# Kernel tuning notes

Measured on AMD Instinct MI355X. Metric: run time of the kernel, lower is better.

The kernel has to match this reference:

```python
import jax, jax.numpy as jnp
import numpy as np

NUM_HEADS = 16
D_MODEL = 1024
TEMPERATURE = D_MODEL ** 0.5  # note: module uses d_model**0.5, not head_dim**0.5


def setup_inputs() -> dict:
    key = jax.random.key(0)
    ks = jax.random.split(key, 8)
    B, T, D = 2, 2048, D_MODEL
    q = jax.random.normal(ks[0], (B, T, D), dtype=jnp.float32)
    k = jax.random.normal(ks[1], (B, T, D), dtype=jnp.float32)
    v = jax.random.normal(ks[2], (B, T, D), dtype=jnp.float32)
    # causal mask (tril) as suggested by the module docstring
    mask = jnp.tril(jnp.ones((T, T), dtype=bool))
    s = 1.0 / np.sqrt(D)
    Wq = jax.random.normal(ks[3], (D, D), dtype=jnp.float32) * s
    Wk = jax.random.normal(ks[4], (D, D), dtype=jnp.float32) * s
    Wv = jax.random.normal(ks[5], (D, D), dtype=jnp.float32) * s
    Wc = jax.random.normal(ks[6], (D, D), dtype=jnp.float32) * s
    return {"q": q, "k": k, "v": v, "Wq": Wq, "Wk": Wk, "Wv": Wv, "Wc": Wc, "mask": mask}


def reference(q, k, v, Wq, Wk, Wv, Wc, mask):
    B, T, D = q.shape
    H = NUM_HEADS
    hd = D // H
    # torch Linear (no bias): y = x @ W.T ; then split heads -> [B,H,T,hd]
    def proj(x, W):
        return (x @ W.T).reshape(B, T, H, hd).transpose(0, 2, 1, 3)
    qh, kh, vh = proj(q, Wq), proj(k, Wk), proj(v, Wv)
    # scores [B,H,T,T]
    scores = jnp.einsum("bhqd,bhkd->bhqk", qh / TEMPERATURE, kh)
    scores = jnp.where(mask, scores, -jnp.inf)
    attention = jax.nn.softmax(scores, axis=-1)  # dropout = identity (eval)
    out = jnp.einsum("bhqk,bhkd->bhqd", attention, vh)
    out = out.transpose(0, 2, 1, 3).reshape(B, T, D)
    out = out @ Wc.T  # combine projection; dropout = identity (eval)
    return (out, attention)
```

## Files before the change

kernel.cpp:

```cpp
#include <hip/hip_runtime.h>
#include <stdint.h>

typedef unsigned short u16;
typedef __bf16 bf16x8 __attribute__((ext_vector_type(8)));
typedef float f32x4 __attribute__((ext_vector_type(4)));

#define MFMA16(a, b, c) __builtin_amdgcn_mfma_f32_16x16x32_bf16((a), (b), (c), 0, 0, 0)

__device__ __forceinline__ u16 f2bf(float f) {
  union { __bf16 h; u16 u; } v;
  v.h = (__bf16)f;
  return v.u;
}

__device__ __forceinline__ float expf_c(float x) {
  return __expf(fmaxf(x, -80.0f));
}

struct Cvt6Args {
  const float* s0; const float* s1; const float* s2;
  const float* s3; const float* s4; const float* s5;
  u16* d0; u16* d1; u16* d2; u16* d3; u16* d4; u16* d5;
};

__global__ __launch_bounds__(256) void cvt6(Cvt6Args a) {
  const int z = blockIdx.y;
  const float* s; u16* d; int n8;
  if (z == 0)      { s = a.s0; d = a.d0; n8 = (4 * 1024 * 1024) / 8; }
  else if (z == 1) { s = a.s1; d = a.d1; n8 = (4 * 1024 * 1024) / 8; }
  else if (z == 2) { s = a.s2; d = a.d2; n8 = (4 * 1024 * 1024) / 8; }
  else if (z == 3) { s = a.s3; d = a.d3; n8 = (1024 * 1024) / 8; }
  else if (z == 4) { s = a.s4; d = a.d4; n8 = (1024 * 1024) / 8; }
  else             { s = a.s5; d = a.d5; n8 = (1024 * 1024) / 8; }
  const int i = blockIdx.x * 256 + threadIdx.x;
  if (i >= n8) return;
  float4 f0 = ((const float4*)s)[2 * i];
  float4 f1 = ((const float4*)s)[2 * i + 1];
  ushort4 h0, h1;
  h0.x = f2bf(f0.x); h0.y = f2bf(f0.y); h0.z = f2bf(f0.z); h0.w = f2bf(f0.w);
  h1.x = f2bf(f1.x); h1.y = f2bf(f1.y); h1.z = f2bf(f1.z); h1.w = f2bf(f1.w);
  ((ushort4*)d)[2 * i] = h0;
  ((ushort4*)d)[2 * i + 1] = h1;
}

__global__ __launch_bounds__(256) void cvt_one(const float* __restrict__ s,
                                               u16* __restrict__ d) {
  const int i = blockIdx.x * 256 + threadIdx.x;
  if (i >= (1024 * 1024) / 8) return;
  float4 f0 = ((const float4*)s)[2 * i];
  float4 f1 = ((const float4*)s)[2 * i + 1];
  ushort4 h0, h1;
  h0.x = f2bf(f0.x); h0.y = f2bf(f0.y); h0.z = f2bf(f0.z); h0.w = f2bf(f0.w);
  h1.x = f2bf(f1.x); h1.y = f2bf(f1.y); h1.z = f2bf(f1.z); h1.w = f2bf(f1.w);
  ((ushort4*)d)[2 * i] = h0;
  ((ushort4*)d)[2 * i + 1] = h1;
}

__device__ __forceinline__ void gemm_core(const u16* __restrict__ X,
                                          const u16* __restrict__ W,
                                          void* __restrict__ Yv, float scale,
                                          int omode) {
  __shared__ __align__(16) u16 lA[128 * 40];
  __shared__ __align__(16) u16 lB[128 * 40];
  const int tid = threadIdx.x;
  const int lane = tid & 63, w = tid >> 6;
  const int l15 = lane & 15, quad = lane >> 4;
  const int wm = (w >> 1) * 64, wn = (w & 1) * 64;
  const int m0 = blockIdx.x * 128, n0 = blockIdx.y * 128;

  f32x4 acc[4][4];
#pragma unroll
  for (int m = 0; m < 4; ++m)
#pragma unroll
    for (int n = 0; n < 4; ++n) acc[m][n] = (f32x4){0.f, 0.f, 0.f, 0.f};

  const int brow = tid >> 2, bseg = (tid & 3) * 8;

  for (int kk = 0; kk < 1024; kk += 32) {
    __syncthreads();
#pragma unroll
    for (int p = 0; p < 2; ++p) {
      int row = p * 64 + brow;
      *(uint4*)&lA[row * 40 + bseg] =
          *(const uint4*)&X[(size_t)(m0 + row) * 1024 + kk + bseg];
      *(uint4*)&lB[row * 40 + bseg] =
          *(const uint4*)&W[(size_t)(n0 + row) * 1024 + kk + bseg];
    }
    __syncthreads();
    bf16x8 af[4], bfr[4];
#pragma unroll
    for (int m = 0; m < 4; ++m)
      af[m] = *(const bf16x8*)&lA[(wm + m * 16 + l15) * 40 + quad * 8];
#pragma unroll
    for (int n = 0; n < 4; ++n)
      bfr[n] = *(const bf16x8*)&lB[(wn + n * 16 + l15) * 40 + quad * 8];
#pragma unroll
    for (int m = 0; m < 4; ++m)
#pragma unroll
      for (int n = 0; n < 4; ++n) acc[m][n] = MFMA16(af[m], bfr[n], acc[m][n]);
  }

  if (omode == 0) {
    u16* Y = (u16*)Yv;
#pragma unroll
    for (int m = 0; m < 4; ++m) {
      int grow0 = m0 + wm + m * 16 + quad * 4;
#pragma unroll
      for (int n = 0; n < 4; ++n) {
        int gcol = n0 + wn + n * 16 + l15;
#pragma unroll
        for (int r = 0; r < 4; ++r)
          Y[(size_t)(grow0 + r) * 1024 + gcol] = f2bf(acc[m][n][r] * scale);
      }
    }
  } else if (omode == 1) {
    u16* Y = (u16*)Yv;
#pragma unroll
    for (int m = 0; m < 4; ++m) {
      int grow0 = m0 + wm + m * 16 + quad * 4;
      int bb = grow0 >> 11, t = grow0 & 2047;
#pragma unroll
      for (int n = 0; n < 4; ++n) {
        int gcol = n0 + wn + n * 16 + l15;
        int hh = gcol >> 6, e = gcol & 63;
        ushort4 pk;
        pk.x = f2bf(acc[m][n][0]);
        pk.y = f2bf(acc[m][n][1]);
        pk.z = f2bf(acc[m][n][2]);
        pk.w = f2bf(acc[m][n][3]);
        *(ushort4*)&Y[((size_t)((bb * 16 + hh) * 64 + e)) * 2048 + t] = pk;
      }
    }
  } else {
    float* Y = (float*)Yv;
#pragma unroll
    for (int m = 0; m < 4; ++m) {
      int grow0 = m0 + wm + m * 16 + quad * 4;
#pragma unroll
      for (int n = 0; n < 4; ++n) {
        int gcol = n0 + wn + n * 16 + l15;
#pragma unroll
        for (int r = 0; r < 4; ++r)
          Y[(size_t)(grow0 + r) * 1024 + gcol] = acc[m][n][r] * scale;
      }
    }
  }
}

struct QKVArgs {
  const u16* X0; const u16* X1; const u16* X2;
  const u16* W0; const u16* W1; const u16* W2;
  void* Y0; void* Y1; void* Y2;
  float s0, s1, s2;
};

__global__ __launch_bounds__(256, 2) void proj_qkv(QKVArgs a) {
  const u16* X; const u16* W; void* Y; float sc; int om;
  if (blockIdx.z == 0)      { X = a.X0; W = a.W0; Y = a.Y0; sc = a.s0; om = 0; }
  else if (blockIdx.z == 1) { X = a.X1; W = a.W1; Y = a.Y1; sc = a.s1; om = 0; }
  else                      { X = a.X2; W = a.W2; Y = a.Y2; sc = a.s2; om = 1; }
  gemm_core(X, W, Y, sc, om);
}

__global__ __launch_bounds__(256, 2) void proj_out(const u16* __restrict__ Xv,
                                                   const u16* __restrict__ W,
                                                   void* __restrict__ Yv) {
  gemm_core(Xv, W, Yv, 1.0f, 2);
}

__global__ __launch_bounds__(256, 3) void attn_kernel(const u16* Qb,
                                                      const u16* __restrict__ Kb,
                                                      const u16* __restrict__ Vt,
                                                      float* __restrict__ attnF,
                                                      u16* Ob,
                                                      float* __restrict__ rowInv) {
  __shared__ __align__(16) u16 lK[64 * 72];
  __shared__ __align__(16) u16 lV[64 * 72];
  __shared__ __align__(16) u16 lP[4][16 * 72];

  const int bid = blockIdx.x;
  const int qt = bid & 31, bh = bid >> 5;
  const int b = bh >> 4, h = bh & 15;
  const int q0 = qt * 64;
  const int tid = threadIdx.x;
  const int w = tid >> 6, lane = tid & 63;
  const int l15 = lane & 15, quad = lane >> 4;

  {
    const int kz0 = q0 + 64;
    if (kz0 < 2048) {
      int r = tid >> 2;
      size_t base = ((size_t)bh * 2048 + q0 + r) * 2048;
      uint4 z = {0, 0, 0, 0};
      for (int c = kz0 + (tid & 3) * 4; c < 2048; c += 16)
        *(uint4*)&attnF[base + c] = z;
    }
  }

  const size_t qrowbase = (size_t)(b * 2048 + q0 + w * 16 + l15) * 1024 + h * 64;
  const bf16x8 aq0 = *(const bf16x8*)&Qb[qrowbase + quad * 8];
  const bf16x8 aq1 = *(const bf16x8*)&Qb[qrowbase + 32 + quad * 8];

  const int qglob0 = q0 + w * 16 + quad * 4;
  const int srow = tid >> 3, sseg = (tid & 7) * 8;

  float lpart[4];
  f32x4 o[4];
#pragma unroll
  for (int i = 0; i < 4; ++i) lpart[i] = 0.f;
#pragma unroll
  for (int n = 0; n < 4; ++n) o[n] = (f32x4){0.f, 0.f, 0.f, 0.f};

  size_t arow[4];
#pragma unroll
  for (int i = 0; i < 4; ++i)
    arow[i] = ((size_t)bh * 2048 + qglob0 + i) * 2048;

  for (int c = 0; c <= qt; ++c) {
    const int k0 = c * 64;
    __syncthreads();
#pragma unroll
    for (int p = 0; p < 2; ++p) {
      int rr = p * 32 + srow;
      *(uint4*)&lK[rr * 72 + sseg] =
          *(const uint4*)&Kb[(size_t)(b * 2048 + k0 + rr) * 1024 + h * 64 + sseg];
      *(uint4*)&lV[rr * 72 + sseg] =
          *(const uint4*)&Vt[((size_t)bh * 64 + rr) * 2048 + k0 + sseg];
    }
    __syncthreads();
    f32x4 s[4];
#pragma unroll
    for (int n = 0; n < 4; ++n) {
      s[n] = (f32x4){0.f, 0.f, 0.f, 0.f};
      bf16x8 bk0 = *(const bf16x8*)&lK[(n * 16 + l15) * 72 + quad * 8];
      bf16x8 bk1 = *(const bf16x8*)&lK[(n * 16 + l15) * 72 + 32 + quad * 8];
      s[n] = MFMA16(aq0, bk0, s[n]);
      s[n] = MFMA16(aq1, bk1, s[n]);
    }
    const bool diag = (c == qt);
#pragma unroll
    for (int n = 0; n < 4; ++n) {
      int key = k0 + n * 16 + l15;
#pragma unroll
      for (int i = 0; i < 4; ++i) {
        float p = expf_c(s[n][i]);
        if (diag && key > qglob0 + i) p = 0.f;
        lpart[i] += p;
        lP[w][(quad * 4 + i) * 72 + n * 16 + l15] = f2bf(p);
        attnF[arow[i] + key] = p;
      }
    }
#pragma unroll
    for (int kkk = 0; kkk < 2; ++kkk) {
      bf16x8 ap = *(const bf16x8*)&lP[w][l15 * 72 + kkk * 32 + quad * 8];
#pragma unroll
      for (int n = 0; n < 4; ++n) {
        bf16x8 bv = *(const bf16x8*)&lV[(n * 16 + l15) * 72 + kkk * 32 + quad * 8];
        o[n] = MFMA16(ap, bv, o[n]);
      }
    }
  }

  float invl[4];
#pragma unroll
  for (int i = 0; i < 4; ++i) {
    float l = lpart[i];
#pragma unroll
    for (int off = 1; off < 16; off <<= 1) l += __shfl_xor(l, off);
    invl[i] = 1.0f / fmaxf(l, 1e-30f);
    if (l15 == 0) rowInv[bh * 2048 + qglob0 + i] = invl[i];
  }

#pragma unroll
  for (int n = 0; n < 4; ++n)
#pragma unroll
    for (int i = 0; i < 4; ++i) {
      float ov = o[n][i] * invl[i];
      if (!(ov == ov)) ov = 0.f;
      lP[w][(quad * 4 + i) * 72 + n * 16 + l15] = f2bf(ov);
    }
  {
    int prow = lane >> 3, pseg = (lane & 7) * 8;
#pragma unroll
    for (int p2 = 0; p2 < 2; ++p2) {
      int rr = p2 * 8 + prow;
      *(uint4*)&Ob[(size_t)(b * 2048 + q0 + w * 16 + rr) * 1024 + h * 64 + pseg] =
          *(const uint4*)&lP[w][rr * 72 + pseg];
    }
  }
}

__global__ __launch_bounds__(256) void rescale_attn(float* __restrict__ attnF,
                                                    const float* __restrict__ rowInv) {
  const int bh = blockIdx.x;
  const int pg = blockIdx.y;
  const int pr = threadIdx.x >> 4;
  const int ln = threadIdx.x & 15;
  const int rp = pg * 16 + pr;
  const size_t bhbase = (size_t)bh * 2048 * 2048;
#pragma unroll
  for (int sel = 0; sel < 2; ++sel) {
    const int t = sel ? (2047 - rp) : rp;
    const float inv = rowInv[bh * 2048 + t];
    float* row = attnF + bhbase + (size_t)t * 2048;
    const int end = t + 1;
    for (int c = ln * 4; c < end; c += 64) {
      float4 p = *(float4*)&row[c];
      p.x *= inv; p.y *= inv; p.z *= inv; p.w *= inv;
      *(float4*)&row[c] = p;
    }
  }
}

extern "C" void kernel_launch(void* const* d_in, const int* in_sizes, int n_in,
                              void* d_out, int out_size, void* d_ws, size_t ws_size,
                              hipStream_t stream) {
  const float* q  = (const float*)d_in[0];
  const float* k  = (const float*)d_in[1];
  const float* v  = (const float*)d_in[2];
  const float* Wq = (const float*)d_in[3];
  const float* Wk = (const float*)d_in[4];
  const float* Wv = (const float*)d_in[5];
  const float* Wc = (const float*)d_in[6];

  float* outF  = (float*)d_out;
  float* attnF = outF + (size_t)4096 * 1024;

  const size_t BUF  = (size_t)4096 * 1024;
  const size_t WBUF = (size_t)1024 * 1024;
  const size_t INVL_BYTES = (size_t)65536 * sizeof(float);
  u16* ws = (u16*)d_ws;
  const bool big_ws = ws_size >= 4 * BUF * sizeof(u16) + INVL_BYTES;

  u16 *Qb, *Kb, *Vt, *Ob;
  float* rowInv;
  if (big_ws) {
    Qb = ws; Kb = ws + BUF; Vt = ws + 2 * BUF; Ob = ws + 3 * BUF;
    rowInv = (float*)(ws + 4 * BUF);
  } else {
    Qb = (u16*)outF; Ob = (u16*)outF + BUF; Kb = ws; Vt = ws + BUF;
    rowInv = (float*)(ws + 2 * BUF);
  }

  u16* qbf  = (u16*)attnF;
  u16* kbf  = qbf  + BUF;
  u16* vbf  = kbf  + BUF;
  u16* wqbf = vbf  + BUF;
  u16* wkbf = wqbf + WBUF;
  u16* wvbf = wkbf + WBUF;
  u16* wcbf = Vt;

  dim3 blk(256, 1, 1);

  Cvt6Args ca;
  ca.s0 = q;    ca.s1 = k;    ca.s2 = v;
  ca.s3 = Wq;   ca.s4 = Wk;   ca.s5 = Wv;
  ca.d0 = qbf;  ca.d1 = kbf;  ca.d2 = vbf;
  ca.d3 = wqbf; ca.d4 = wkbf; ca.d5 = wvbf;
  cvt6<<<dim3(2048, 6), blk, 0, stream>>>(ca);

  QKVArgs a;
  a.X0 = qbf;  a.X1 = kbf;  a.X2 = vbf;
  a.W0 = wqbf; a.W1 = wkbf; a.W2 = wvbf;
  a.Y0 = Qb; a.Y1 = Kb; a.Y2 = Vt;
  a.s0 = 0.03125f;
  a.s1 = 1.0f; a.s2 = 1.0f;
  proj_qkv<<<dim3(32, 8, 3), blk, 0, stream>>>(a);
  attn_kernel<<<dim3(1024), blk, 0, stream>>>(Qb, Kb, Vt, attnF, Ob, rowInv);

  cvt_one<<<dim3(512), blk, 0, stream>>>(Wc, wcbf);

  const u16* gemm_src = Ob;
  if (!big_ws) {
    hipMemcpyAsync(ws, Ob, BUF * sizeof(u16), hipMemcpyDeviceToDevice, stream);
    gemm_src = ws;
  }
  proj_out<<<dim3(32, 8), blk, 0, stream>>>(gemm_src, wcbf, outF);
  rescale_attn<<<dim3(32, 64), blk, 0, stream>>>(attnF, rowInv);
}
```

Before: 906.1 us.

## Two-pass attention: compute row sums first, write normalized probabilities directly

The attention kernel now makes a first pass over the causal key tiles to compute the softmax denominators, then a second pass that recomputes the scores and writes already-normalized probabilities. This removes the separate rescale kernel, which re-read and re-wrote the whole lower-triangular attention matrix. The QK MFMA operands are swapped so each lane holds four consecutive keys of one query row, enabling float4 stores to the attention output. K and V tiles are now read directly from global memory instead of being staged in LDS, which drops the block barriers but may increase global traffic and doubles the QK compute.

```diff
diff --git a/kernel.cpp b/kernel.cpp
--- a/kernel.cpp
+++ b/kernel.cpp
@@ -168,14 +168,11 @@
   gemm_core(Xv, W, Yv, 1.0f, 2);
 }
 
-__global__ __launch_bounds__(256, 3) void attn_kernel(const u16* Qb,
+__global__ __launch_bounds__(256, 3) void attn_kernel(const u16* __restrict__ Qb,
                                                       const u16* __restrict__ Kb,
                                                       const u16* __restrict__ Vt,
                                                       float* __restrict__ attnF,
-                                                      u16* Ob,
-                                                      float* __restrict__ rowInv) {
-  __shared__ __align__(16) u16 lK[64 * 72];
-  __shared__ __align__(16) u16 lV[64 * 72];
+                                                      u16* __restrict__ Ob) {
   __shared__ __align__(16) u16 lP[4][16 * 72];
 
   const int bid = blockIdx.x;
@@ -185,6 +182,7 @@
   const int tid = threadIdx.x;
   const int w = tid >> 6, lane = tid & 63;
   const int l15 = lane & 15, quad = lane >> 4;
+  const f32x4 ZERO4 = {0.f, 0.f, 0.f, 0.f};
 
   {
     const int kz0 = q0 + 64;
@@ -197,87 +195,97 @@
     }
   }
 
-  const size_t qrowbase = (size_t)(b * 2048 + q0 + w * 16 + l15) * 1024 + h * 64;
+  const int qrow = q0 + w * 16 + l15;
+  const size_t qrowbase = (size_t)(b * 2048 + qrow) * 1024 + h * 64;
   const bf16x8 aq0 = *(const bf16x8*)&Qb[qrowbase + quad * 8];
   const bf16x8 aq1 = *(const bf16x8*)&Qb[qrowbase + 32 + quad * 8];
 
-  const int qglob0 = q0 + w * 16 + quad * 4;
-  const int srow = tid >> 3, sseg = (tid & 7) * 8;
-
-  float lpart[4];
-  f32x4 o[4];
-#pragma unroll
-  for (int i = 0; i < 4; ++i) lpart[i] = 0.f;
-#pragma unroll
-  for (int n = 0; n < 4; ++n) o[n] = (f32x4){0.f, 0.f, 0.f, 0.f};
-
-  size_t arow[4];
-#pragma unroll
-  for (int i = 0; i < 4; ++i)
-    arow[i] = ((size_t)bh * 2048 + qglob0 + i) * 2048;
-
+  const int kq = quad * 4;
+  const size_t kb_base = (size_t)b * 2048 * 1024 + h * 64;
+
+  float lacc = 0.f;
   for (int c = 0; c <= qt; ++c) {
     const int k0 = c * 64;
-    __syncthreads();
-#pragma unroll
-    for (int p = 0; p < 2; ++p) {
-      int rr = p * 32 + srow;
-      *(uint4*)&lK[rr * 72 + sseg] =
-          *(const uint4*)&Kb[(size_t)(b * 2048 + k0 + rr) * 1024 + h * 64 + sseg];
-      *(uint4*)&lV[rr * 72 + sseg] =
-          *(const uint4*)&Vt[((size_t)bh * 64 + rr) * 2048 + k0 + sseg];
-    }
-    __syncthreads();
     f32x4 s[4];
 #pragma unroll
     for (int n = 0; n < 4; ++n) {
-      s[n] = (f32x4){0.f, 0.f, 0.f, 0.f};
-      bf16x8 bk0 = *(const bf16x8*)&lK[(n * 16 + l15) * 72 + quad * 8];
-      bf16x8 bk1 = *(const bf16x8*)&lK[(n * 16 + l15) * 72 + 32 + quad * 8];
-      s[n] = MFMA16(aq0, bk0, s[n]);
-      s[n] = MFMA16(aq1, bk1, s[n]);
+      const size_t krow = kb_base + (size_t)(k0 + n * 16 + l15) * 1024;
+      bf16x8 bk0 = *(const bf16x8*)&Kb[krow + quad * 8];
+      bf16x8 bk1 = *(const bf16x8*)&Kb[krow + 32 + quad * 8];
+      s[n] = MFMA16(bk0, aq0, ZERO4);
+      s[n] = MFMA16(bk1, aq1, s[n]);
+    }
+    if (c == qt) {
+#pragma unroll
+      for (int n = 0; n < 4; ++n) {
+        const int keyb = k0 + n * 16 + kq;
+#pragma unroll
+        for (int i = 0; i < 4; ++i)
+          lacc += (keyb + i > qrow) ? 0.f : expf_c(s[n][i]);
+      }
+    } else {
+#pragma unroll
+      for (int n = 0; n < 4; ++n)
+#pragma unroll
+        for (int i = 0; i < 4; ++i) lacc += expf_c(s[n][i]);
+    }
+  }
+  lacc += __shfl_xor(lacc, 16);
+  lacc += __shfl_xor(lacc, 32);
+  const float invl = 1.0f / fmaxf(lacc, 1e-30f);
+
+  f32x4 o[4];
+#pragma unroll
+  for (int n = 0; n < 4; ++n) o[n] = ZERO4;
+  const size_t arow = ((size_t)bh * 2048 + qrow) * 2048;
+  u16* lPw = lP[w];
+
+  for (int c = 0; c <= qt; ++c) {
+    const int k0 = c * 64;
+    f32x4 s[4];
+#pragma unroll
+    for (int n = 0; n < 4; ++n) {
+      const size_t krow = kb_base + (size_t)(k0 + n * 16 + l15) * 1024;
+      bf16x8 bk0 = *(const bf16x8*)&Kb[krow + quad * 8];
+      bf16x8 bk1 = *(const bf16x8*)&Kb[krow + 32 + quad * 8];
+      s[n] = MFMA16(bk0, aq0, ZERO4);
+      s[n] = MFMA16(bk1, aq1, s[n]);
     }
     const bool diag = (c == qt);
 #pragma unroll
     for (int n = 0; n < 4; ++n) {
-      int key = k0 + n * 16 + l15;
+      const int keyb = k0 + n * 16 + kq;
 #pragma unroll
       for (int i = 0; i < 4; ++i) {
-        float p = expf_c(s[n][i]);
-        if (diag && key > qglob0 + i) p = 0.f;
-        lpart[i] += p;
-        lP[w][(quad * 4 + i) * 72 + n * 16 + l15] = f2bf(p);
-        attnF[arow[i] + key] = p;
-      }
+        float p = expf_c(s[n][i]) * invl;
+        if (diag && keyb + i > qrow) p = 0.f;
+        s[n][i] = p;
+      }
+      *(f32x4*)&attnF[arow + keyb] = s[n];
+      ushort4 pk;
+      pk.x = f2bf(s[n][0]); pk.y = f2bf(s[n][1]);
+      pk.z = f2bf(s[n][2]); pk.w = f2bf(s[n][3]);
+      *(ushort4*)&lPw[l15 * 72 + n * 16 + kq] = pk;
     }
 #pragma unroll
     for (int kkk = 0; kkk < 2; ++kkk) {
-      bf16x8 ap = *(const bf16x8*)&lP[w][l15 * 72 + kkk * 32 + quad * 8];
-#pragma unroll
-      for (int n = 0; n < 4; ++n) {
-        bf16x8 bv = *(const bf16x8*)&lV[(n * 16 + l15) * 72 + kkk * 32 + quad * 8];
+      bf16x8 ap = *(const bf16x8*)&lPw[l15 * 72 + kkk * 32 + quad * 8];
+#pragma unroll
+      for (int n = 0; n < 4; ++n) {
+        const size_t vrow = ((size_t)(bh * 64 + n * 16 + l15)) * 2048;
+        bf16x8 bv = *(const bf16x8*)&Vt[vrow + k0 + kkk * 32 + quad * 8];
         o[n] = MFMA16(ap, bv, o[n]);
       }
     }
   }
 
-  float invl[4];
-#pragma unroll
-  for (int i = 0; i < 4; ++i) {
-    float l = lpart[i];
-#pragma unroll
-    for (int off = 1; off < 16; off <<= 1) l += __shfl_xor(l, off);
-    invl[i] = 1.0f / fmaxf(l, 1e-30f);
-    if (l15 == 0) rowInv[bh * 2048 + qglob0 + i] = invl[i];
-  }
-
 #pragma unroll
   for (int n = 0; n < 4; ++n)
 #pragma unroll
     for (int i = 0; i < 4; ++i) {
-      float ov = o[n][i] * invl[i];
+      float ov = o[n][i];
       if (!(ov == ov)) ov = 0.f;
-      lP[w][(quad * 4 + i) * 72 + n * 16 + l15] = f2bf(ov);
+      lPw[(quad * 4 + i) * 72 + n * 16 + l15] = f2bf(ov);
     }
   {
     int prow = lane >> 3, pseg = (lane & 7) * 8;
@@ -285,29 +293,7 @@
     for (int p2 = 0; p2 < 2; ++p2) {
       int rr = p2 * 8 + prow;
       *(uint4*)&Ob[(size_t)(b * 2048 + q0 + w * 16 + rr) * 1024 + h * 64 + pseg] =
-          *(const uint4*)&lP[w][rr * 72 + pseg];
-    }
-  }
-}
-
-__global__ __launch_bounds__(256) void rescale_attn(float* __restrict__ attnF,
-                                                    const float* __restrict__ rowInv) {
-  const int bh = blockIdx.x;
-  const int pg = blockIdx.y;
-  const int pr = threadIdx.x >> 4;
-  const int ln = threadIdx.x & 15;
-  const int rp = pg * 16 + pr;
-  const size_t bhbase = (size_t)bh * 2048 * 2048;
-#pragma unroll
-  for (int sel = 0; sel < 2; ++sel) {
-    const int t = sel ? (2047 - rp) : rp;
-    const float inv = rowInv[bh * 2048 + t];
-    float* row = attnF + bhbase + (size_t)t * 2048;
-    const int end = t + 1;
-    for (int c = ln * 4; c < end; c += 64) {
-      float4 p = *(float4*)&row[c];
-      p.x *= inv; p.y *= inv; p.z *= inv; p.w *= inv;
-      *(float4*)&row[c] = p;
+          *(const uint4*)&lPw[rr * 72 + pseg];
     }
   }
 }
@@ -328,18 +314,14 @@
 
   const size_t BUF  = (size_t)4096 * 1024;
   const size_t WBUF = (size_t)1024 * 1024;
-  const size_t INVL_BYTES = (size_t)65536 * sizeof(float);
   u16* ws = (u16*)d_ws;
-  const bool big_ws = ws_size >= 4 * BUF * sizeof(u16) + INVL_BYTES;
+  const bool big_ws = ws_size >= 4 * BUF * sizeof(u16);
 
   u16 *Qb, *Kb, *Vt, *Ob;
-  float* rowInv;
   if (big_ws) {
     Qb = ws; Kb = ws + BUF; Vt = ws + 2 * BUF; Ob = ws + 3 * BUF;
-    rowInv = (float*)(ws + 4 * BUF);
   } else {
     Qb = (u16*)outF; Ob = (u16*)outF + BUF; Kb = ws; Vt = ws + BUF;
-    rowInv = (float*)(ws + 2 * BUF);
   }
 
   u16* qbf  = (u16*)attnF;
@@ -366,15 +348,14 @@
   a.s0 = 0.03125f;
   a.s1 = 1.0f; a.s2 = 1.0f;
   proj_qkv<<<dim3(32, 8, 3), blk, 0, stream>>>(a);
-  attn_kernel<<<dim3(1024), blk, 0, stream>>>(Qb, Kb, Vt, attnF, Ob, rowInv);
+  attn_kernel<<<dim3(1024), blk, 0, stream>>>(Qb, Kb, Vt, attnF, Ob);
 
   cvt_one<<<dim3(512), blk, 0, stream>>>(Wc, wcbf);
 
   const u16* gemm_src = Ob;
   if (!big_ws) {
-    hipMemcpyAsync(ws, Ob, BUF * sizeof(u16), hipMemcpyDeviceToDevice, stream);
+    (void)hipMemcpyAsync(ws, Ob, BUF * sizeof(u16), hipMemcpyDeviceToDevice, stream);
     gemm_src = ws;
   }
   proj_out<<<dim3(32, 8), blk, 0, stream>>>(gemm_src, wcbf, outF);
-  rescale_attn<<<dim3(32, 64), blk, 0, stream>>>(attnF, rowInv);
-}
+}
```

After: 969.5 us. +7.0%, slower.
